# Optimization experiments

Hardware: AMD Instinct MI355X
Metric: run time of the kernel (lower is better)

The kernel has to match this reference:

```python
import jax, jax.numpy as jnp
import numpy as np

K = 3
PAD = 1
STRIDE = 1
DIL = 1


def _conv_offset(x, w, b):
    # standard 3x3 conv, NCHW
    out = jax.lax.conv_general_dilated(
        x, w, window_strides=(STRIDE, STRIDE), padding=((PAD, PAD), (PAD, PAD)),
        rhs_dilation=(DIL, DIL), dimension_numbers=('NCHW', 'OIHW', 'NCHW'))
    return out + b[None, :, None, None]


def _bilinear_sample(x, px, py):
    # x: (b,c,h,w); px,py: (b,N) absolute pixel coords; zero padding outside.
    b, c, h, w = x.shape
    x_flat = x.reshape(b, c, h * w)
    x0 = jnp.floor(px)
    y0 = jnp.floor(py)
    wx1 = px - x0
    wy1 = py - y0
    wx0 = 1.0 - wx1
    wy0 = 1.0 - wy1

    def gather(xi, yi, wt):
        valid = (xi >= 0) & (xi <= w - 1) & (yi >= 0) & (yi <= h - 1)
        xc = jnp.clip(xi, 0, w - 1).astype(jnp.int32)
        yc = jnp.clip(yi, 0, h - 1).astype(jnp.int32)
        idx = yc * w + xc  # (b,N)
        v = jax.vmap(lambda xf, i: jnp.take(xf, i, axis=1))(x_flat, idx)  # (b,c,N)
        return v * (wt * valid.astype(x.dtype))[:, None, :]

    out = gather(x0, y0, wy0 * wx0)
    out = out + gather(x0 + 1, y0, wy0 * wx1)
    out = out + gather(x0, y0 + 1, wy1 * wx0)
    out = out + gather(x0 + 1, y0 + 1, wy1 * wx1)
    return out


def setup_inputs() -> dict:
    key = jax.random.key(0)
    k1, k2, k3, k4 = jax.random.split(key, 4)
    x = jax.random.normal(k1, (8, 64, 128, 128), dtype=jnp.float32)
    # small random offset-predictor weights (repo inits to zero; random gives nonzero offsets)
    w_off = jax.random.normal(k2, (27, 64, 3, 3), dtype=jnp.float32) * 0.01
    b_off = jax.random.normal(k3, (27,), dtype=jnp.float32) * 0.01
    w_conv = jax.random.normal(k4, (64, 576), dtype=jnp.float32) / np.sqrt(3.0 * 576.0)
    return {"x": x, "w_off": w_off, "b_off": b_off, "w_conv": w_conv}


def reference(x, w_off, b_off, w_conv):
    b, c, h, w = x.shape
    out = _conv_offset(x, w_off, b_off)  # (b, 3*K*K, H, W)
    H, W = out.shape[2], out.shape[3]
    o1, o2, m = jnp.split(out, 3, axis=1)  # each (b, K*K, H, W)
    mask = jax.nn.sigmoid(m).reshape(b, 1, K, K, H, W)
    # base grid (absolute coords), per module __init__
    x_start = DIL / 2 * (K - 1) - PAD  # = 0.0 here
    y_start = DIL / 2 * (K - 1) - PAD
    x_cood = (x_start + STRIDE * jnp.arange(W)).astype(x.dtype)
    y_cood = (y_start + STRIDE * jnp.arange(H)).astype(x.dtype)
    # per-tap kernel bias, tap order is (kh, kw) row-major
    taps = (jnp.arange(K) - (K - 1) / 2) * DIL
    x_bias = jnp.tile(taps, K).astype(x.dtype)      # (K*K,)
    y_bias = jnp.repeat(taps, K).astype(x.dtype)    # (K*K,)
    px = o1 + x_cood[None, None, None, :] + x_bias[None, :, None, None]  # (b,9,H,W)
    py = o2 + y_cood[None, None, :, None] + y_bias[None, :, None, None]
    N = K * K * H * W
    y = _bilinear_sample(x, px.reshape(b, N), py.reshape(b, N))  # (b,c,N)
    y = y.reshape(b, c, K, K, H, W) * mask
    y = y.reshape(b, c * K * K, H, W)
    # 1x1 conv == channel GEMM
    return jnp.einsum('bkhw,ok->bohw', y, w_conv)
```

## Files before the change

kernel.cpp:

```cpp
#include <hip/hip_runtime.h>
#include <math.h>

#define HW_   128
#define CIN_  64
#define IMG_  (HW_ * HW_)

#define TR_    5
#define TC_    72
#define PIT_   36
#define TILEDW (TR_ * TC_ * PIT_)

typedef short    s16x8 __attribute__((ext_vector_type(8)));
typedef float    f32x4 __attribute__((ext_vector_type(4)));
typedef float    f32x2 __attribute__((ext_vector_type(2)));
typedef unsigned u32x4 __attribute__((ext_vector_type(4)));

__device__ __forceinline__ short f2bf(float f) {
  union { float f; unsigned i; } v; v.f = f;
  unsigned r = (v.i + 0x7fffu + ((v.i >> 16) & 1u)) >> 16;
  return (short)r;
}

#if defined(__has_builtin)
#if __has_builtin(__builtin_amdgcn_cvt_pk_bf16_f32)
#define HAVE_CVT_PK_BF16 1
#endif
#endif

__device__ __forceinline__ unsigned PK2(float a, float b) {
#ifdef HAVE_CVT_PK_BF16
  typedef __bf16 bf16x2_t __attribute__((ext_vector_type(2)));
  union { bf16x2_t v; unsigned u; } cv;
  cv.v = __builtin_amdgcn_cvt_pk_bf16_f32(a, b);
  return cv.u;
#else
  union { float f; unsigned u; } ua, ub; ua.f = a; ub.f = b;
  unsigned ra = ua.u + 0x7fffu + ((ua.u >> 16) & 1u);
  unsigned rb = ub.u + 0x7fffu + ((ub.u >> 16) & 1u);
  return __builtin_amdgcn_perm(rb, ra, 0x07060302u);
#endif
}
__device__ __forceinline__ f32x2 up2(unsigned d) {
  union { unsigned u; float f; } lo, hi;
  lo.u = d << 16; hi.u = d & 0xffff0000u;
  return (f32x2){lo.f, hi.f};
}


__global__ __launch_bounds__(256) void wprep(const float* __restrict__ w_off,
                                             const float* __restrict__ w_conv,
                                             short* __restrict__ wOf,
                                             short* __restrict__ wA) {
  int t = blockIdx.x * 256 + threadIdx.x;
  if (t < 36864) {
    int i = t & 7, o = (t >> 3) & 63, q = (t >> 9) & 3, ks = (t >> 11) & 1, j = t >> 12;
    int c = ks * 32 + q * 8 + i;
    wA[t] = f2bf(w_conv[o * 576 + c * 9 + j]);
  }
  if (t < 18432) {
    int i = t & 7, m = (t >> 3) & 31, q = (t >> 8) & 3, ks = (t >> 10) & 1, j = t >> 11;
    int c = ks * 32 + q * 8 + i;
    wOf[t] = (m < 27) ? f2bf(w_off[(m * 64 + c) * 9 + j]) : (short)0;
  }
}

__global__ __launch_bounds__(256)
__attribute__((amdgpu_waves_per_eu(3)))
void dfuse(const float* __restrict__ x,
           const short* __restrict__ wOf,
           const float* __restrict__ b_off,
           const short* __restrict__ wA,
           float* __restrict__ out) {
  __shared__ __align__(16) unsigned lds_[TILEDW];

  int bi  = blockIdx.x >> 8;
  int hw0 = (blockIdx.x & 255) * 64;
  int h   = hw0 >> 7;
  int w0  = hw0 & 127;
  int t   = threadIdx.x;
  int wv  = t >> 6, l = t & 63;
  int col = l & 15, q = l >> 4;
  int px_local = wv * 16 + col;
  int p = hw0 + px_local;
  int w = w0 + px_local;

  const float* xB = x + (size_t)bi * (CIN_ * IMG_);

  for (int u = t; u < TR_ * 32 * 18; u += 256) {
    int cc = u % 18;
    int rc = u / 18;
    int cp = rc & 31;
    int r  = rc >> 5;
    int y  = h - 2 + r;
    int ys = min(max(y, 0), HW_ - 1);
    int xg0 = w0 - 4 + cc * 4;
    int xs  = min(max(xg0, 0), HW_ - 4);
    const float* s0 = xB + (2 * cp) * IMG_ + ys * HW_ + xs;
    float4 f0 = *(const float4*)s0;
    float4 f1 = *(const float4*)(s0 + IMG_);
    int sd = ((ys - (h - 2)) * TC_ + (xs - (w0 - 4))) * PIT_ + cp;
    lds_[sd]            = PK2(f0.x, f1.x);
    lds_[sd + PIT_]     = PK2(f0.y, f1.y);
    lds_[sd + 2 * PIT_] = PK2(f0.z, f1.z);
    lds_[sd + 3 * PIT_] = PK2(f0.w, f1.w);
  }
  __syncthreads();

  float oall[32];
  {
    const short* wq = wOf + q * 256 + col * 8;
    f32x4 a0v = {0.f, 0.f, 0.f, 0.f};
    f32x4 a1v = {0.f, 0.f, 0.f, 0.f};
#pragma unroll
    for (int j = 0; j < 9; ++j) {
      int dy = j / 3 - 1, dx = j % 3 - 1;
      int hh = h + dy, ww = w + dx;
      unsigned m = (hh >= 0 && hh < HW_ && ww >= 0 && ww < HW_) ? 0xffffffffu : 0u;
      const unsigned* tp = &lds_[((dy + 2) * TC_ + (px_local + dx + 4)) * PIT_ + q * 4];
      u32x4 b0u = *(const u32x4*)tp;
      u32x4 b1u = *(const u32x4*)(tp + 16);
#pragma unroll
      for (int i = 0; i < 4; ++i) { b0u[i] &= m; b1u[i] &= m; }
      union { u32x4 u; s16x8 v; } B0, B1;
      B0.u = b0u; B1.u = b1u;
      const short* wj = wq + j * 2048;
      s16x8 a00 = *(const s16x8*)(wj);
      s16x8 a01 = *(const s16x8*)(wj + 128);
      s16x8 a10 = *(const s16x8*)(wj + 1024);
      s16x8 a11 = *(const s16x8*)(wj + 1024 + 128);
      a0v = __builtin_amdgcn_mfma_f32_16x16x32_bf16(a00, B0.v, a0v, 0, 0, 0);
      a1v = __builtin_amdgcn_mfma_f32_16x16x32_bf16(a01, B0.v, a1v, 0, 0, 0);
      a0v = __builtin_amdgcn_mfma_f32_16x16x32_bf16(a10, B1.v, a0v, 0, 0, 0);
      a1v = __builtin_amdgcn_mfma_f32_16x16x32_bf16(a11, B1.v, a1v, 0, 0, 0);
    }
    float myv[8];
#pragma unroll
    for (int r = 0; r < 4; ++r) myv[r] = a0v[r] + b_off[q * 4 + r];
#pragma unroll
    for (int r = 0; r < 4; ++r) {
      int ch = 16 + q * 4 + r;
      float bo = b_off[min(ch, 26)];
      float v = a1v[r] + bo;
      myv[4 + r] = (ch >= 18) ? (1.f / (1.f + __expf(-v))) : v;
    }
#pragma unroll
    for (int qq = 0; qq < 4; ++qq) {
      int src = qq * 16 + col;
#pragma unroll
      for (int r = 0; r < 4; ++r) {
        oall[qq * 4 + r]      = __shfl(myv[r], src);
        oall[16 + qq * 4 + r] = __shfl(myv[4 + r], src);
      }
    }
  }

  f32x4 acc[4];
#pragma unroll
  for (int ms = 0; ms < 4; ++ms) acc[ms] = (f32x4){0.f, 0.f, 0.f, 0.f};

  const short* wq = wA + q * 512 + col * 8;

#pragma unroll
  for (int j = 0; j < 9; ++j) {
    float o1 = oall[j], o2 = oall[9 + j], mk = oall[18 + j];

    float pxf = o1 + (float)(w + (j % 3) - 1);
    float pyf = o2 + (float)(h + (j / 3) - 1);
    float fx = floorf(pxf), fy = floorf(pyf);
    int   x0 = (int)fx,   y0 = (int)fy;
    float ax = pxf - fx, ay = pyf - fy;
    float bx = 1.f - ax, by = 1.f - ay;

    bool vx0 = (x0 >= 0)  && (x0 < HW_);
    bool vx1 = (x0 >= -1) && (x0 < HW_ - 1);
    bool vy0 = (y0 >= 0)  && (y0 < HW_);
    bool vy1 = (y0 >= -1) && (y0 < HW_ - 1);

    float u00 = by * bx * mk * ((vy0 && vx0) ? 1.f : 0.f);
    float u01 = by * ax * mk * ((vy0 && vx1) ? 1.f : 0.f);
    float u10 = ay * bx * mk * ((vy1 && vx0) ? 1.f : 0.f);
    float u11 = ay * ax * mk * ((vy1 && vx1) ? 1.f : 0.f);

    int xc0 = min(max(x0, 0), HW_ - 1), xc1 = min(max(x0 + 1, 0), HW_ - 1);
    int yc0 = min(max(y0, 0), HW_ - 1), yc1 = min(max(y0 + 1, 0), HW_ - 1);

    unsigned F0u[4], F1u[4];
    bool intile = (o1 >= -1.f) && (o1 < 1.f) && (o2 >= -1.f) && (o2 < 1.f);
    if (intile) {
      int r0 = yc0 - (h - 2),  r1 = yc1 - (h - 2);
      int c0 = xc0 - (w0 - 4), c1 = xc1 - (w0 - 4);
      const unsigned* t00 = &lds_[(r0 * TC_ + c0) * PIT_ + q * 4];
      const unsigned* t01 = &lds_[(r0 * TC_ + c1) * PIT_ + q * 4];
      const unsigned* t10 = &lds_[(r1 * TC_ + c0) * PIT_ + q * 4];
      const unsigned* t11 = &lds_[(r1 * TC_ + c1) * PIT_ + q * 4];
      u32x4 A00 = *(const u32x4*)t00, B00 = *(const u32x4*)(t00 + 16);
      u32x4 A01 = *(const u32x4*)t01, B01 = *(const u32x4*)(t01 + 16);
      u32x4 A10 = *(const u32x4*)t10, B10 = *(const u32x4*)(t10 + 16);
      u32x4 A11 = *(const u32x4*)t11, B11 = *(const u32x4*)(t11 + 16);
#pragma unroll
      for (int i = 0; i < 4; ++i) {
        f32x2 v0 = up2(A00[i]) * u00;
        v0 += up2(A01[i]) * u01;
        v0 += up2(A10[i]) * u10;
        v0 += up2(A11[i]) * u11;
        F0u[i] = PK2(v0.x, v0.y);
        f32x2 v1 = up2(B00[i]) * u00;
        v1 += up2(B01[i]) * u01;
        v1 += up2(B10[i]) * u10;
        v1 += up2(B11[i]) * u11;
        F1u[i] = PK2(v1.x, v1.y);
      }
    } else {
      int g00 = yc0 * HW_ + xc0, g01 = yc0 * HW_ + xc1;
      int g10 = yc1 * HW_ + xc0, g11 = yc1 * HW_ + xc1;
      for (int hB = 0; hB < 2; ++hB) {
        for (int ii = 0; ii < 4; ++ii) {
          int c0 = hB * 32 + q * 8 + 2 * ii;
          const float* pc = xB + c0 * IMG_;
          const float* pd = pc + IMG_;
          float va = u00 * pc[g00] + u01 * pc[g01] + u10 * pc[g10] + u11 * pc[g11];
          float vb = u00 * pd[g00] + u01 * pd[g01] + u10 * pd[g10] + u11 * pd[g11];
          if (hB) F1u[ii] = PK2(va, vb); else F0u[ii] = PK2(va, vb);
        }
      }
    }

    union { unsigned u[4]; s16x8 v; } F0, F1;
#pragma unroll
    for (int i = 0; i < 4; ++i) { F0.u[i] = F0u[i]; F1.u[i] = F1u[i]; }

    const short* wj = wq + j * 4096;
#pragma unroll
    for (int ms = 0; ms < 4; ++ms) {
      s16x8 a0 = *(const s16x8*)(wj + ms * 128);
      acc[ms] = __builtin_amdgcn_mfma_f32_16x16x32_bf16(a0, F0.v, acc[ms], 0, 0, 0);
    }
#pragma unroll
    for (int ms = 0; ms < 4; ++ms) {
      s16x8 a1 = *(const s16x8*)(wj + 2048 + ms * 128);
      acc[ms] = __builtin_amdgcn_mfma_f32_16x16x32_bf16(a1, F1.v, acc[ms], 0, 0, 0);
    }
  }

  float* op = out + (size_t)bi * (CIN_ * IMG_) + p;
#pragma unroll
  for (int ms = 0; ms < 4; ++ms)
#pragma unroll
    for (int r = 0; r < 4; ++r)
      op[(ms * 16 + q * 4 + r) * IMG_] = acc[ms][r];
}

extern "C" void kernel_launch(void* const* d_in, const int* in_sizes, int n_in,
                              void* d_out, int out_size, void* d_ws, size_t ws_size,
                              hipStream_t stream) {
  const float* x      = (const float*)d_in[0];
  const float* w_off  = (const float*)d_in[1];
  const float* b_off  = (const float*)d_in[2];
  const float* w_conv = (const float*)d_in[3];
  float* out = (float*)d_out;

  char* ws = (char*)d_ws;
  short* wOf = (short*)(ws);
  short* wA  = (short*)(ws + 36864);

  hipLaunchKernelGGL(wprep, dim3(144),  dim3(256), 0, stream, w_off, w_conv, wOf, wA);
  hipLaunchKernelGGL(dfuse, dim3(2048), dim3(256), 0, stream, x, wOf, b_off, wA, out);
}
```

Baseline: 146.8 us.

## Zero-pad LDS halo, use odd pitch, and simplify bilinear sampling math

The staged input tile is now written at fixed tile coordinates, with out-of-image halo entries zero-filled. This lets the offset conv drop its per-tap boundary masks, and lets the in-tile bilinear path index unclamped coordinates from a single base pointer. The LDS channel pitch changes from 36 to 35 dwords to spread accesses across banks. The corner weights are built with fewer multiplies, and the bf16 blend uses scalar fmas. The odd pitch breaks 16-byte alignment of the vector LDS reads, which may force the compiler to split them into smaller loads.

```diff
diff --git a/kernel.cpp b/kernel.cpp
--- a/kernel.cpp
+++ b/kernel.cpp
@@ -7,12 +7,11 @@
 
 #define TR_    5
 #define TC_    72
-#define PIT_   36
+#define PIT_   35
 #define TILEDW (TR_ * TC_ * PIT_)
 
 typedef short    s16x8 __attribute__((ext_vector_type(8)));
 typedef float    f32x4 __attribute__((ext_vector_type(4)));
-typedef float    f32x2 __attribute__((ext_vector_type(2)));
 typedef unsigned u32x4 __attribute__((ext_vector_type(4)));
 
 __device__ __forceinline__ short f2bf(float f) {
@@ -40,10 +39,12 @@
   return __builtin_amdgcn_perm(rb, ra, 0x07060302u);
 #endif
 }
-__device__ __forceinline__ f32x2 up2(unsigned d) {
-  union { unsigned u; float f; } lo, hi;
-  lo.u = d << 16; hi.u = d & 0xffff0000u;
-  return (f32x2){lo.f, hi.f};
+
+__device__ __forceinline__ float bfl(unsigned d) {
+  union { unsigned u; float f; } v; v.u = d << 16; return v.f;
+}
+__device__ __forceinline__ float bfh(unsigned d) {
+  union { unsigned u; float f; } v; v.u = d; return v.f;
 }
 
 
@@ -95,14 +96,15 @@
     int ys = min(max(y, 0), HW_ - 1);
     int xg0 = w0 - 4 + cc * 4;
     int xs  = min(max(xg0, 0), HW_ - 4);
+    bool ok = (y >= 0) && (y < HW_) && (xg0 >= 0) && (xg0 < HW_);
     const float* s0 = xB + (2 * cp) * IMG_ + ys * HW_ + xs;
     float4 f0 = *(const float4*)s0;
     float4 f1 = *(const float4*)(s0 + IMG_);
-    int sd = ((ys - (h - 2)) * TC_ + (xs - (w0 - 4))) * PIT_ + cp;
-    lds_[sd]            = PK2(f0.x, f1.x);
-    lds_[sd + PIT_]     = PK2(f0.y, f1.y);
-    lds_[sd + 2 * PIT_] = PK2(f0.z, f1.z);
-    lds_[sd + 3 * PIT_] = PK2(f0.w, f1.w);
+    int sd = (r * TC_ + cc * 4) * PIT_ + cp;
+    lds_[sd]            = ok ? PK2(f0.x, f1.x) : 0u;
+    lds_[sd + PIT_]     = ok ? PK2(f0.y, f1.y) : 0u;
+    lds_[sd + 2 * PIT_] = ok ? PK2(f0.z, f1.z) : 0u;
+    lds_[sd + 3 * PIT_] = ok ? PK2(f0.w, f1.w) : 0u;
   }
   __syncthreads();
 
@@ -111,18 +113,14 @@
     const short* wq = wOf + q * 256 + col * 8;
     f32x4 a0v = {0.f, 0.f, 0.f, 0.f};
     f32x4 a1v = {0.f, 0.f, 0.f, 0.f};
+    const unsigned* tb = &lds_[(px_local + 4) * PIT_ + q * 4];
 #pragma unroll
     for (int j = 0; j < 9; ++j) {
       int dy = j / 3 - 1, dx = j % 3 - 1;
-      int hh = h + dy, ww = w + dx;
-      unsigned m = (hh >= 0 && hh < HW_ && ww >= 0 && ww < HW_) ? 0xffffffffu : 0u;
-      const unsigned* tp = &lds_[((dy + 2) * TC_ + (px_local + dx + 4)) * PIT_ + q * 4];
-      u32x4 b0u = *(const u32x4*)tp;
-      u32x4 b1u = *(const u32x4*)(tp + 16);
-#pragma unroll
-      for (int i = 0; i < 4; ++i) { b0u[i] &= m; b1u[i] &= m; }
+      const unsigned* tp = tb + ((dy + 2) * TC_ + dx) * PIT_;
       union { u32x4 u; s16x8 v; } B0, B1;
-      B0.u = b0u; B1.u = b1u;
+      B0.u = *(const u32x4*)tp;
+      B1.u = *(const u32x4*)(tp + 16);
       const short* wj = wq + j * 2048;
       s16x8 a00 = *(const s16x8*)(wj);
       s16x8 a01 = *(const s16x8*)(wj + 128);
@@ -158,7 +156,7 @@
 #pragma unroll
   for (int ms = 0; ms < 4; ++ms) acc[ms] = (f32x4){0.f, 0.f, 0.f, 0.f};
 
-  const short* wq = wA + q * 512 + col * 8;
+  const short* wqA = wA + q * 512 + col * 8;
 
 #pragma unroll
   for (int j = 0; j < 9; ++j) {
@@ -171,52 +169,49 @@
     float ax = pxf - fx, ay = pyf - fy;
     float bx = 1.f - ax, by = 1.f - ay;
 
-    bool vx0 = (x0 >= 0)  && (x0 < HW_);
-    bool vx1 = (x0 >= -1) && (x0 < HW_ - 1);
-    bool vy0 = (y0 >= 0)  && (y0 < HW_);
-    bool vy1 = (y0 >= -1) && (y0 < HW_ - 1);
-
-    float u00 = by * bx * mk * ((vy0 && vx0) ? 1.f : 0.f);
-    float u01 = by * ax * mk * ((vy0 && vx1) ? 1.f : 0.f);
-    float u10 = ay * bx * mk * ((vy1 && vx0) ? 1.f : 0.f);
-    float u11 = ay * ax * mk * ((vy1 && vx1) ? 1.f : 0.f);
-
-    int xc0 = min(max(x0, 0), HW_ - 1), xc1 = min(max(x0 + 1, 0), HW_ - 1);
-    int yc0 = min(max(y0, 0), HW_ - 1), yc1 = min(max(y0 + 1, 0), HW_ - 1);
+    bx = (x0 >= 0  && x0 < HW_)     ? bx : 0.f;
+    ax = (x0 >= -1 && x0 < HW_ - 1) ? ax : 0.f;
+    by = (y0 >= 0  && y0 < HW_)     ? by : 0.f;
+    ay = (y0 >= -1 && y0 < HW_ - 1) ? ay : 0.f;
+    float bym = by * mk, aym = ay * mk;
+    float u00 = bym * bx, u01 = bym * ax;
+    float u10 = aym * bx, u11 = aym * ax;
 
     unsigned F0u[4], F1u[4];
     bool intile = (o1 >= -1.f) && (o1 < 1.f) && (o2 >= -1.f) && (o2 < 1.f);
     if (intile) {
-      int r0 = yc0 - (h - 2),  r1 = yc1 - (h - 2);
-      int c0 = xc0 - (w0 - 4), c1 = xc1 - (w0 - 4);
+      int r0 = y0 - (h - 2), c0 = x0 - (w0 - 4);
       const unsigned* t00 = &lds_[(r0 * TC_ + c0) * PIT_ + q * 4];
-      const unsigned* t01 = &lds_[(r0 * TC_ + c1) * PIT_ + q * 4];
-      const unsigned* t10 = &lds_[(r1 * TC_ + c0) * PIT_ + q * 4];
-      const unsigned* t11 = &lds_[(r1 * TC_ + c1) * PIT_ + q * 4];
-      u32x4 A00 = *(const u32x4*)t00, B00 = *(const u32x4*)(t00 + 16);
-      u32x4 A01 = *(const u32x4*)t01, B01 = *(const u32x4*)(t01 + 16);
-      u32x4 A10 = *(const u32x4*)t10, B10 = *(const u32x4*)(t10 + 16);
-      u32x4 A11 = *(const u32x4*)t11, B11 = *(const u32x4*)(t11 + 16);
+      u32x4 A00 = *(const u32x4*)(t00);
+      u32x4 A01 = *(const u32x4*)(t00 + PIT_);
+      u32x4 A10 = *(const u32x4*)(t00 + TC_ * PIT_);
+      u32x4 A11 = *(const u32x4*)(t00 + TC_ * PIT_ + PIT_);
+      u32x4 B00 = *(const u32x4*)(t00 + 16);
+      u32x4 B01 = *(const u32x4*)(t00 + PIT_ + 16);
+      u32x4 B10 = *(const u32x4*)(t00 + TC_ * PIT_ + 16);
+      u32x4 B11 = *(const u32x4*)(t00 + TC_ * PIT_ + PIT_ + 16);
 #pragma unroll
       for (int i = 0; i < 4; ++i) {
-        f32x2 v0 = up2(A00[i]) * u00;
-        v0 += up2(A01[i]) * u01;
-        v0 += up2(A10[i]) * u10;
-        v0 += up2(A11[i]) * u11;
-        F0u[i] = PK2(v0.x, v0.y);
-        f32x2 v1 = up2(B00[i]) * u00;
-        v1 += up2(B01[i]) * u01;
-        v1 += up2(B10[i]) * u10;
-        v1 += up2(B11[i]) * u11;
-        F1u[i] = PK2(v1.x, v1.y);
+        float vlo = fmaf(bfl(A00[i]), u00, fmaf(bfl(A01[i]), u01,
+                    fmaf(bfl(A10[i]), u10, bfl(A11[i]) * u11)));
+        float vhi = fmaf(bfh(A00[i]), u00, fmaf(bfh(A01[i]), u01,
+                    fmaf(bfh(A10[i]), u10, bfh(A11[i]) * u11)));
+        F0u[i] = PK2(vlo, vhi);
+        float wlo = fmaf(bfl(B00[i]), u00, fmaf(bfl(B01[i]), u01,
+                    fmaf(bfl(B10[i]), u10, bfl(B11[i]) * u11)));
+        float whi = fmaf(bfh(B00[i]), u00, fmaf(bfh(B01[i]), u01,
+                    fmaf(bfh(B10[i]), u10, bfh(B11[i]) * u11)));
+        F1u[i] = PK2(wlo, whi);
       }
     } else {
+      int xc0 = min(max(x0, 0), HW_ - 1), xc1 = min(max(x0 + 1, 0), HW_ - 1);
+      int yc0 = min(max(y0, 0), HW_ - 1), yc1 = min(max(y0 + 1, 0), HW_ - 1);
       int g00 = yc0 * HW_ + xc0, g01 = yc0 * HW_ + xc1;
       int g10 = yc1 * HW_ + xc0, g11 = yc1 * HW_ + xc1;
       for (int hB = 0; hB < 2; ++hB) {
         for (int ii = 0; ii < 4; ++ii) {
-          int c0 = hB * 32 + q * 8 + 2 * ii;
-          const float* pc = xB + c0 * IMG_;
+          int c0i = hB * 32 + q * 8 + 2 * ii;
+          const float* pc = xB + c0i * IMG_;
           const float* pd = pc + IMG_;
           float va = u00 * pc[g00] + u01 * pc[g01] + u10 * pc[g10] + u11 * pc[g11];
           float vb = u00 * pd[g00] + u01 * pd[g01] + u10 * pd[g10] + u11 * pd[g11];
@@ -229,7 +224,7 @@
 #pragma unroll
     for (int i = 0; i < 4; ++i) { F0.u[i] = F0u[i]; F1.u[i] = F1u[i]; }
 
-    const short* wj = wq + j * 4096;
+    const short* wj = wqA + j * 4096;
 #pragma unroll
     for (int ms = 0; ms < 4; ++ms) {
       s16x8 a0 = *(const s16x8*)(wj + ms * 128);
```

Measured after the change: 180.3 us. +22.9%, slower.
